# Performance work log

Measured on AMD Instinct MI355X. Metric: run time of the kernel, lower is better.

The kernel has to match this reference:

```python
import jax, jax.numpy as jnp
import numpy as np

B, S, D, KC = 32, 4096, 64, 256  # batch*heads, seq_len, head_dim, compressed dim


def setup_inputs() -> dict:
    key = jax.random.key(0)
    ks = jax.random.split(key, 7)
    return {
        "Q": jax.random.normal(ks[0], (B, S, D), dtype=jnp.float32),
        "K": jax.random.normal(ks[1], (B, S, D), dtype=jnp.float32),
        "V": jax.random.normal(ks[2], (B, S, D), dtype=jnp.float32),
        "E_w": jax.random.normal(ks[3], (KC, S), dtype=jnp.float32) * (1.0 / np.sqrt(S)),
        "E_b": jax.random.normal(ks[4], (KC,), dtype=jnp.float32) * 0.01,
        "F_w": jax.random.normal(ks[5], (KC, S), dtype=jnp.float32) * (1.0 / np.sqrt(S)),
        "F_b": jax.random.normal(ks[6], (KC,), dtype=jnp.float32) * 0.01,
    }


def reference(Q, K, V, E_w, E_b, F_w, F_b):
    # K: [B,S,D] -> transpose -> [B,D,S]; E proj over seq axis -> [B,D,KC]
    Ke = jnp.einsum("bsd,ks->bdk", K, E_w) + E_b  # [B, D, KC]
    # scores: Q @ E(K) -> [B, S, KC], scaled by sqrt(head_dim)
    scale = jnp.sqrt(jnp.asarray(D, dtype=Q.dtype))
    P = jnp.einsum("bsd,bdk->bsk", Q, Ke) / scale
    # causal mask: torch.triu(ones(S, KC)) keeps (i, j) where j >= i
    i = jnp.arange(S)[:, None]
    j = jnp.arange(KC)[None, :]
    keep = j >= i  # [S, KC]
    P = jnp.where(keep[None, :, :], P, jnp.asarray(-1e10, dtype=P.dtype))
    P = jax.nn.softmax(P, axis=-1)  # dropout p=0.0 -> identity
    # V: [B,S,D] -> [B,D,S]; F proj -> [B,D,KC]; transpose -> [B,KC,D]
    Vf = jnp.einsum("bsd,ks->bkd", V, F_w) + F_b[None, :, None]  # [B, KC, D]
    out = jnp.einsum("bsk,bkd->bsd", P, Vf)  # [B, S, D]
    return out
```

## Files before the change

kernel.cpp:

```cpp
#include <hip/hip_runtime.h>
#include <hip/hip_bf16.h>
#include <math.h>

#define NB  32
#define NS  4096
#define ND  64
#define NKC 256
#define ASTR 72
#define PBSTR 264
#define VSTR  264

typedef __attribute__((ext_vector_type(8))) short short8;
typedef __attribute__((ext_vector_type(4))) float f32x4;

__device__ __forceinline__ short f2bf(float f) {
    union { float f; unsigned u; } v; v.f = f;
    return (short)((v.u + 0x7FFFu + ((v.u >> 16) & 1u)) >> 16);
}

__global__ __launch_bounds__(256) void prep(
    const float* __restrict__ Ew, const float* __restrict__ Fw,
    float4* __restrict__ zws, short* __restrict__ EwB, short* __restrict__ FwB)
{
    const int gid = blockIdx.x * 256 + threadIdx.x;
    zws[gid] = (float4){0.f, 0.f, 0.f, 0.f};

    const int half = (NKC * NS) / 8;
    const float* src = (gid < half) ? Ew : Fw;
    short* dst       = (gid < half) ? EwB : FwB;
    const int i8 = (gid < half) ? gid : gid - half;
    float4 a = *(const float4*)&src[(size_t)i8 * 8];
    float4 c = *(const float4*)&src[(size_t)i8 * 8 + 4];
    short8 w;
    w[0] = f2bf(a.x); w[1] = f2bf(a.y); w[2] = f2bf(a.z); w[3] = f2bf(a.w);
    w[4] = f2bf(c.x); w[5] = f2bf(c.y); w[6] = f2bf(c.z); w[7] = f2bf(c.w);
    *(short8*)&dst[(size_t)i8 * 8] = w;
}

template <typename AT>
__global__ __launch_bounds__(256) void proj_gemm(
    const AT* __restrict__ EwX, const AT* __restrict__ FwX,
    const float* __restrict__ K, const float* __restrict__ V,
    float* __restrict__ KeT, float* __restrict__ Vf)
{
    const int x = blockIdx.x, b = blockIdx.y;
    const int chunk = x >> 1, mm = x & 1;
    const AT* __restrict__ Ab    = mm ? FwX : EwX;
    const float* __restrict__ Bg = mm ? V   : K;
    float* __restrict__ Cout     = mm ? Vf  : KeT;

    const int t = threadIdx.x, wave = t >> 6, lane = t & 63;
    const int lm = lane & 15, g = lane >> 4;
    __shared__ short As[256 * ASTR];
    __shared__ short Bs[64 * ASTR];
    const size_t bBase = (size_t)b * NS * ND;
    const int rA = t >> 3, jA = t & 7;
    const int dB = t & 31, sB = t >> 5;

    f32x4 acc[4][4];
#pragma unroll
    for (int mt = 0; mt < 4; ++mt)
#pragma unroll
        for (int nt = 0; nt < 4; ++nt) acc[mt][nt] = (f32x4){0.f, 0.f, 0.f, 0.f};

    const int sBeg = chunk * 512, sEnd = sBeg + 512;
    short8 pa[8];
    float4 paf[16];
    float2 pb[8];
#pragma unroll
    for (int i = 0; i < 8; ++i) {
        if constexpr (sizeof(AT) == 2) {
            pa[i] = *(const short8*)&Ab[(size_t)(i * 32 + rA) * NS + sBeg + jA * 8];
        } else {
            paf[2 * i]     = *(const float4*)&Ab[(size_t)(i * 32 + rA) * NS + sBeg + jA * 8];
            paf[2 * i + 1] = *(const float4*)&Ab[(size_t)(i * 32 + rA) * NS + sBeg + jA * 8 + 4];
        }
    }
#pragma unroll
    for (int i = 0; i < 8; ++i)
        pb[i] = *(const float2*)&Bg[bBase + (size_t)(sBeg + sB * 8 + i) * ND + dB * 2];

    for (int s0 = sBeg; s0 < sEnd; s0 += 64) {
#pragma unroll
        for (int i = 0; i < 8; ++i) {
            if constexpr (sizeof(AT) == 2) {
                *(short8*)&As[(i * 32 + rA) * ASTR + jA * 8] = pa[i];
            } else {
                short8 w;
                w[0] = f2bf(paf[2 * i].x);     w[1] = f2bf(paf[2 * i].y);
                w[2] = f2bf(paf[2 * i].z);     w[3] = f2bf(paf[2 * i].w);
                w[4] = f2bf(paf[2 * i + 1].x); w[5] = f2bf(paf[2 * i + 1].y);
                w[6] = f2bf(paf[2 * i + 1].z); w[7] = f2bf(paf[2 * i + 1].w);
                *(short8*)&As[(i * 32 + rA) * ASTR + jA * 8] = w;
            }
        }
        {
            short8 w0, w1;
#pragma unroll
            for (int i = 0; i < 8; ++i) { w0[i] = f2bf(pb[i].x); w1[i] = f2bf(pb[i].y); }
            *(short8*)&Bs[(dB * 2 + 0) * ASTR + sB * 8] = w0;
            *(short8*)&Bs[(dB * 2 + 1) * ASTR + sB * 8] = w1;
        }
        __syncthreads();
        if (s0 + 64 < sEnd) {
#pragma unroll
            for (int i = 0; i < 8; ++i) {
                if constexpr (sizeof(AT) == 2) {
                    pa[i] = *(const short8*)&Ab[(size_t)(i * 32 + rA) * NS + s0 + 64 + jA * 8];
                } else {
                    paf[2 * i]     = *(const float4*)&Ab[(size_t)(i * 32 + rA) * NS + s0 + 64 + jA * 8];
                    paf[2 * i + 1] = *(const float4*)&Ab[(size_t)(i * 32 + rA) * NS + s0 + 64 + jA * 8 + 4];
                }
            }
#pragma unroll
            for (int i = 0; i < 8; ++i)
                pb[i] = *(const float2*)&Bg[bBase + (size_t)(s0 + 64 + sB * 8 + i) * ND + dB * 2];
        }
#pragma unroll
        for (int ks = 0; ks < 64; ks += 32) {
            short8 aF[4];
#pragma unroll
            for (int mt = 0; mt < 4; ++mt)
                aF[mt] = *(const short8*)&As[(mt * 64 + wave * 16 + lm) * ASTR + ks + g * 8];
#pragma unroll
            for (int nt = 0; nt < 4; ++nt) {
                short8 bF = *(const short8*)&Bs[(nt * 16 + lm) * ASTR + ks + g * 8];
#pragma unroll
                for (int mt = 0; mt < 4; ++mt)
                    acc[mt][nt] = __builtin_amdgcn_mfma_f32_16x16x32_bf16(aF[mt], bF, acc[mt][nt], 0, 0, 0);
            }
        }
        __syncthreads();
    }
#pragma unroll
    for (int mt = 0; mt < 4; ++mt)
#pragma unroll
        for (int r = 0; r < 4; ++r) {
            int kc = mt * 64 + wave * 16 + g * 4 + r;
#pragma unroll
            for (int nt = 0; nt < 4; ++nt)
                atomicAdd(&Cout[((size_t)b * NKC + kc) * ND + nt * 16 + lm], acc[mt][nt][r]);
        }
}

__global__ __launch_bounds__(256) void attn_fused(
    const float* __restrict__ Q,  const float* __restrict__ KeT,
    const float* __restrict__ Vf, const float* __restrict__ Eb,
    const float* __restrict__ Fb, float* __restrict__ out)
{
    const int x = blockIdx.x, b = blockIdx.y, t = threadIdx.x;

    if (x >= 8) {
        __shared__ float pq[16][64];
        __shared__ float mv[64];
        const int kg = t >> 4, dq = t & 15;
        float4 s4 = (float4){0.f, 0.f, 0.f, 0.f};
        for (int p = 0; p < 16; ++p) {
            int k = p * 16 + kg;
            float4 v = *(const float4*)&Vf[((size_t)b * NKC + k) * ND + dq * 4];
            float fb = Fb[k];
            s4.x += v.x + fb; s4.y += v.y + fb; s4.z += v.z + fb; s4.w += v.w + fb;
        }
        *(float4*)&pq[kg][dq * 4] = s4;
        __syncthreads();
        if (t < 64) {
            float m = 0.f;
#pragma unroll
            for (int i = 0; i < 16; ++i) m += pq[i][t];
            mv[t] = m * (1.f / 256.f);
        }
        __syncthreads();
        const int r0 = 256 + (x - 8) * 64;
#pragma unroll
        for (int i = 0; i < 4; ++i) {
            int idx = i * 256 + t, row = idx >> 4, q = idx & 15;
            *(float4*)&out[((size_t)b * NS + r0 + row) * ND + q * 4] =
                *(const float4*)&mv[q * 4];
        }
        return;
    }

    const int s0 = x * 32;
    const int wave = t >> 6, lane = t & 63, lm = lane & 15, g = lane >> 4;
    __shared__ short Qs[32 * ASTR];
    __shared__ short PsB[32 * PBSTR];
    __shared__ short VfT[64 * VSTR];
    __shared__ float rsums[32][4];

    {
        int row = t >> 3, dq = t & 7;
        size_t off = ((size_t)b * NS + s0 + row) * ND + dq * 8;
        float4 q0 = *(const float4*)&Q[off], q1 = *(const float4*)&Q[off + 4];
        short8 w;
        w[0] = f2bf(q0.x); w[1] = f2bf(q0.y); w[2] = f2bf(q0.z); w[3] = f2bf(q0.w);
        w[4] = f2bf(q1.x); w[5] = f2bf(q1.y); w[6] = f2bf(q1.z); w[7] = f2bf(q1.w);
        *(short8*)&Qs[row * ASTR + dq * 8] = w;
    }
    {
        const int dB = t & 31, sB = t >> 5;
#pragma unroll
        for (int pass = 0; pass < 4; ++pass) {
            int kb = pass * 64 + sB * 8;
            float2 v[8]; float fb[8];
#pragma unroll
            for (int i = 0; i < 8; ++i) {
                v[i]  = *(const float2*)&Vf[((size_t)b * NKC + kb + i) * ND + dB * 2];
                fb[i] = Fb[kb + i];
            }
            short8 w0, w1;
#pragma unroll
            for (int i = 0; i < 8; ++i) {
                w0[i] = f2bf(v[i].x + fb[i]);
                w1[i] = f2bf(v[i].y + fb[i]);
            }
            *(short8*)&VfT[(dB * 2 + 0) * VSTR + kb] = w0;
            *(short8*)&VfT[(dB * 2 + 1) * VSTR + kb] = w1;
        }
    }
    __syncthreads();

    f32x4 accP[2][4];
#pragma unroll
    for (int rt = 0; rt < 2; ++rt)
#pragma unroll
        for (int kk = 0; kk < 4; ++kk) accP[rt][kk] = (f32x4){0.f, 0.f, 0.f, 0.f};
#pragma unroll
    for (int kk = 0; kk < 4; ++kk) {
        int kt = wave * 4 + kk;
        float ebv = Eb[kt * 16 + lm];
#pragma unroll
        for (int ks2 = 0; ks2 < 2; ++ks2) {
            const float* kp = &KeT[((size_t)b * NKC + kt * 16 + lm) * ND + ks2 * 32 + g * 8];
            float4 c0 = *(const float4*)kp, c1 = *(const float4*)(kp + 4);
            short8 bf;
            bf[0] = f2bf(c0.x + ebv); bf[1] = f2bf(c0.y + ebv);
            bf[2] = f2bf(c0.z + ebv); bf[3] = f2bf(c0.w + ebv);
            bf[4] = f2bf(c1.x + ebv); bf[5] = f2bf(c1.y + ebv);
            bf[6] = f2bf(c1.z + ebv); bf[7] = f2bf(c1.w + ebv);
#pragma unroll
            for (int rt = 0; rt < 2; ++rt) {
                short8 aq = *(const short8*)&Qs[(rt * 16 + lm) * ASTR + ks2 * 32 + g * 8];
                accP[rt][kk] = __builtin_amdgcn_mfma_f32_16x16x32_bf16(aq, bf, accP[rt][kk], 0, 0, 0);
            }
        }
    }
#pragma unroll
    for (int rt = 0; rt < 2; ++rt)
#pragma unroll
        for (int r = 0; r < 4; ++r) {
            float s = 0.f;
            int rowg = s0 + rt * 16 + g * 4 + r;
#pragma unroll
            for (int kk = 0; kk < 4; ++kk) {
                int col = wave * 64 + kk * 16 + lm;
                float e = (col >= rowg) ? __expf(accP[rt][kk][r] * 0.125f) : 0.f;
                accP[rt][kk][r] = e;
                s += e;
            }
#pragma unroll
            for (int off = 1; off <= 8; off <<= 1) s += __shfl_xor(s, off, 64);
            if (lm == 0) rsums[rt * 16 + g * 4 + r][wave] = s;
        }
    __syncthreads();
#pragma unroll
    for (int rt = 0; rt < 2; ++rt)
#pragma unroll
        for (int r = 0; r < 4; ++r) {
            float4 rs = *(const float4*)&rsums[rt * 16 + g * 4 + r][0];
            float inv = 1.f / (rs.x + rs.y + rs.z + rs.w);
#pragma unroll
            for (int kk = 0; kk < 4; ++kk)
                PsB[(rt * 16 + g * 4 + r) * PBSTR + wave * 64 + kk * 16 + lm] =
                    f2bf(accP[rt][kk][r] * inv);
        }
    __syncthreads();

    f32x4 oa[2];
    oa[0] = (f32x4){0.f, 0.f, 0.f, 0.f};
    oa[1] = (f32x4){0.f, 0.f, 0.f, 0.f};
    for (int ks = x; ks < 8; ++ks) {
        short8 bv = *(const short8*)&VfT[(wave * 16 + lm) * VSTR + ks * 32 + g * 8];
#pragma unroll
        for (int rt = 0; rt < 2; ++rt) {
            short8 av = *(const short8*)&PsB[(rt * 16 + lm) * PBSTR + ks * 32 + g * 8];
            oa[rt] = __builtin_amdgcn_mfma_f32_16x16x32_bf16(av, bv, oa[rt], 0, 0, 0);
        }
    }
#pragma unroll
    for (int rt = 0; rt < 2; ++rt)
#pragma unroll
        for (int r = 0; r < 4; ++r)
            out[((size_t)b * NS + s0 + rt * 16 + g * 4 + r) * ND + wave * 16 + lm] = oa[rt][r];
}

extern "C" void kernel_launch(void* const* d_in, const int* in_sizes, int n_in,
                              void* d_out, int out_size, void* d_ws, size_t ws_size,
                              hipStream_t stream) {
    (void)in_sizes; (void)n_in; (void)out_size;
    const float* Q  = (const float*)d_in[0];
    const float* K  = (const float*)d_in[1];
    const float* V  = (const float*)d_in[2];
    const float* Ew = (const float*)d_in[3];
    const float* Eb = (const float*)d_in[4];
    const float* Fw = (const float*)d_in[5];
    const float* Fb = (const float*)d_in[6];
    float* out = (float*)d_out;

    const size_t nKe = (size_t)NB * NKC * ND;
    float* KeT = (float*)d_ws;
    float* Vf  = KeT + nKe;

    if (ws_size >= 8u * 1024 * 1024) {
        short* EwB = (short*)(Vf + nKe);
        short* FwB = EwB + (size_t)NKC * NS;
        prep<<<dim3(1024), 256, 0, stream>>>(Ew, Fw, (float4*)d_ws, EwB, FwB);
        proj_gemm<short><<<dim3(16, NB), 256, 0, stream>>>(EwB, FwB, K, V, KeT, Vf);
    } else {
        hipMemsetAsync(d_ws, 0, 2 * nKe * sizeof(float), stream);
        proj_gemm<float><<<dim3(16, NB), 256, 0, stream>>>(Ew, Fw, K, V, KeT, Vf);
    }
    attn_fused<<<dim3(68, NB), 256, 0, stream>>>(Q, KeT, Vf, Eb, Fb, out);
}
```

Before: 179.3 us.

## Split projection GEMM by M-half and replace atomics with partial-sum reduction

Drops the separate bf16 pre-conversion kernel and memset, converting E_w/F_w to bf16 on the fly inside the projection GEMM. The GEMM grid is doubled by splitting the 256 compressed rows into two halves, and each block writes plain partial sums (staged in the output buffer) instead of issuing atomicAdds. A new reduce kernel sums the 8 sequence-chunk partials into KeT/Vf. This removes atomic contention and a launch, and raises occupancy with launch_bounds(256,4). In exchange it re-reads fp32 weights in every batch block and adds a partial-buffer write/read pass.

New measurement: 181.0 us. Within noise of the previous version (+1.0%).

```diff
diff --git a/kernel.cpp b/kernel.cpp
--- a/kernel.cpp
+++ b/kernel.cpp
@@ -18,63 +18,39 @@
     return (short)((v.u + 0x7FFFu + ((v.u >> 16) & 1u)) >> 16);
 }
 
-__global__ __launch_bounds__(256) void prep(
+__global__ __launch_bounds__(256, 4) void proj_gemm(
     const float* __restrict__ Ew, const float* __restrict__ Fw,
-    float4* __restrict__ zws, short* __restrict__ EwB, short* __restrict__ FwB)
+    const float* __restrict__ K,  const float* __restrict__ V,
+    float* __restrict__ part)
 {
-    const int gid = blockIdx.x * 256 + threadIdx.x;
-    zws[gid] = (float4){0.f, 0.f, 0.f, 0.f};
-
-    const int half = (NKC * NS) / 8;
-    const float* src = (gid < half) ? Ew : Fw;
-    short* dst       = (gid < half) ? EwB : FwB;
-    const int i8 = (gid < half) ? gid : gid - half;
-    float4 a = *(const float4*)&src[(size_t)i8 * 8];
-    float4 c = *(const float4*)&src[(size_t)i8 * 8 + 4];
-    short8 w;
-    w[0] = f2bf(a.x); w[1] = f2bf(a.y); w[2] = f2bf(a.z); w[3] = f2bf(a.w);
-    w[4] = f2bf(c.x); w[5] = f2bf(c.y); w[6] = f2bf(c.z); w[7] = f2bf(c.w);
-    *(short8*)&dst[(size_t)i8 * 8] = w;
-}
-
-template <typename AT>
-__global__ __launch_bounds__(256) void proj_gemm(
-    const AT* __restrict__ EwX, const AT* __restrict__ FwX,
-    const float* __restrict__ K, const float* __restrict__ V,
-    float* __restrict__ KeT, float* __restrict__ Vf)
-{
-    const int x = blockIdx.x, b = blockIdx.y;
+    const int x = blockIdx.x, y = blockIdx.y;
     const int chunk = x >> 1, mm = x & 1;
-    const AT* __restrict__ Ab    = mm ? FwX : EwX;
-    const float* __restrict__ Bg = mm ? V   : K;
-    float* __restrict__ Cout     = mm ? Vf  : KeT;
+    const int b = y >> 1, mhalf = y & 1;
+    const float* __restrict__ A  = (mm ? Fw : Ew) + (size_t)(mhalf * 128) * NS;
+    const float* __restrict__ Bg = mm ? V : K;
+    float* __restrict__ Pout = part + ((size_t)x * 32 + b) * 16384 + mhalf * 8192;
 
     const int t = threadIdx.x, wave = t >> 6, lane = t & 63;
     const int lm = lane & 15, g = lane >> 4;
-    __shared__ short As[256 * ASTR];
+    __shared__ short As[128 * ASTR];
     __shared__ short Bs[64 * ASTR];
     const size_t bBase = (size_t)b * NS * ND;
     const int rA = t >> 3, jA = t & 7;
     const int dB = t & 31, sB = t >> 5;
 
-    f32x4 acc[4][4];
-#pragma unroll
-    for (int mt = 0; mt < 4; ++mt)
+    f32x4 acc[2][4];
+#pragma unroll
+    for (int mt = 0; mt < 2; ++mt)
 #pragma unroll
         for (int nt = 0; nt < 4; ++nt) acc[mt][nt] = (f32x4){0.f, 0.f, 0.f, 0.f};
 
     const int sBeg = chunk * 512, sEnd = sBeg + 512;
-    short8 pa[8];
-    float4 paf[16];
+    float4 paf[8];
     float2 pb[8];
 #pragma unroll
-    for (int i = 0; i < 8; ++i) {
-        if constexpr (sizeof(AT) == 2) {
-            pa[i] = *(const short8*)&Ab[(size_t)(i * 32 + rA) * NS + sBeg + jA * 8];
-        } else {
-            paf[2 * i]     = *(const float4*)&Ab[(size_t)(i * 32 + rA) * NS + sBeg + jA * 8];
-            paf[2 * i + 1] = *(const float4*)&Ab[(size_t)(i * 32 + rA) * NS + sBeg + jA * 8 + 4];
-        }
+    for (int i = 0; i < 4; ++i) {
+        paf[2 * i]     = *(const float4*)&A[(size_t)(i * 32 + rA) * NS + sBeg + jA * 8];
+        paf[2 * i + 1] = *(const float4*)&A[(size_t)(i * 32 + rA) * NS + sBeg + jA * 8 + 4];
     }
 #pragma unroll
     for (int i = 0; i < 8; ++i)
@@ -82,17 +58,13 @@
 
     for (int s0 = sBeg; s0 < sEnd; s0 += 64) {
 #pragma unroll
-        for (int i = 0; i < 8; ++i) {
-            if constexpr (sizeof(AT) == 2) {
-                *(short8*)&As[(i * 32 + rA) * ASTR + jA * 8] = pa[i];
-            } else {
-                short8 w;
-                w[0] = f2bf(paf[2 * i].x);     w[1] = f2bf(paf[2 * i].y);
-                w[2] = f2bf(paf[2 * i].z);     w[3] = f2bf(paf[2 * i].w);
-                w[4] = f2bf(paf[2 * i + 1].x); w[5] = f2bf(paf[2 * i + 1].y);
-                w[6] = f2bf(paf[2 * i + 1].z); w[7] = f2bf(paf[2 * i + 1].w);
-                *(short8*)&As[(i * 32 + rA) * ASTR + jA * 8] = w;
-            }
+        for (int i = 0; i < 4; ++i) {
+            short8 w;
+            w[0] = f2bf(paf[2 * i].x);     w[1] = f2bf(paf[2 * i].y);
+            w[2] = f2bf(paf[2 * i].z);     w[3] = f2bf(paf[2 * i].w);
+            w[4] = f2bf(paf[2 * i + 1].x); w[5] = f2bf(paf[2 * i + 1].y);
+            w[6] = f2bf(paf[2 * i + 1].z); w[7] = f2bf(paf[2 * i + 1].w);
+            *(short8*)&As[(i * 32 + rA) * ASTR + jA * 8] = w;
         }
         {
             short8 w0, w1;
@@ -104,13 +76,9 @@
         __syncthreads();
         if (s0 + 64 < sEnd) {
 #pragma unroll
-            for (int i = 0; i < 8; ++i) {
-                if constexpr (sizeof(AT) == 2) {
-                    pa[i] = *(const short8*)&Ab[(size_t)(i * 32 + rA) * NS + s0 + 64 + jA * 8];
-                } else {
-                    paf[2 * i]     = *(const float4*)&Ab[(size_t)(i * 32 + rA) * NS + s0 + 64 + jA * 8];
-                    paf[2 * i + 1] = *(const float4*)&Ab[(size_t)(i * 32 + rA) * NS + s0 + 64 + jA * 8 + 4];
-                }
+            for (int i = 0; i < 4; ++i) {
+                paf[2 * i]     = *(const float4*)&A[(size_t)(i * 32 + rA) * NS + s0 + 64 + jA * 8];
+                paf[2 * i + 1] = *(const float4*)&A[(size_t)(i * 32 + rA) * NS + s0 + 64 + jA * 8 + 4];
             }
 #pragma unroll
             for (int i = 0; i < 8; ++i)
@@ -118,29 +86,54 @@
         }
 #pragma unroll
         for (int ks = 0; ks < 64; ks += 32) {
-            short8 aF[4];
-#pragma unroll
-            for (int mt = 0; mt < 4; ++mt)
+            short8 aF[2];
+#pragma unroll
+            for (int mt = 0; mt < 2; ++mt)
                 aF[mt] = *(const short8*)&As[(mt * 64 + wave * 16 + lm) * ASTR + ks + g * 8];
 #pragma unroll
             for (int nt = 0; nt < 4; ++nt) {
                 short8 bF = *(const short8*)&Bs[(nt * 16 + lm) * ASTR + ks + g * 8];
 #pragma unroll
-                for (int mt = 0; mt < 4; ++mt)
+                for (int mt = 0; mt < 2; ++mt)
                     acc[mt][nt] = __builtin_amdgcn_mfma_f32_16x16x32_bf16(aF[mt], bF, acc[mt][nt], 0, 0, 0);
             }
         }
         __syncthreads();
     }
 #pragma unroll
-    for (int mt = 0; mt < 4; ++mt)
+    for (int mt = 0; mt < 2; ++mt)
 #pragma unroll
         for (int r = 0; r < 4; ++r) {
-            int kc = mt * 64 + wave * 16 + g * 4 + r;
+            int kcl = mt * 64 + wave * 16 + g * 4 + r;
 #pragma unroll
             for (int nt = 0; nt < 4; ++nt)
-                atomicAdd(&Cout[((size_t)b * NKC + kc) * ND + nt * 16 + lm], acc[mt][nt][r]);
-        }
+                Pout[kcl * 64 + nt * 16 + lm] = acc[mt][nt][r];
+        }
+}
+
+__global__ __launch_bounds__(256) void reduce_part(
+    const float* __restrict__ part, float* __restrict__ KeT, float* __restrict__ Vf)
+{
+    const int x = blockIdx.x, y = blockIdx.y, t = threadIdx.x;
+    const int b = y >> 1, mm = y & 1;
+    float* __restrict__ Out = (mm ? Vf : KeT) + (size_t)b * NKC * ND;
+
+    const int kc = x * 32 + (t >> 3);
+    const int dO = (t & 7) * 8;
+    const int mhalf = kc >> 7, kcl = kc & 127;
+    const size_t inner = (size_t)mhalf * 8192 + kcl * 64 + dO;
+
+    float4 s0 = (float4){0.f, 0.f, 0.f, 0.f};
+    float4 s1 = (float4){0.f, 0.f, 0.f, 0.f};
+#pragma unroll
+    for (int c = 0; c < 8; ++c) {
+        const float* p = part + ((size_t)(c * 2 + mm) * 32 + b) * 16384 + inner;
+        float4 a = *(const float4*)p, bb = *(const float4*)(p + 4);
+        s0.x += a.x;  s0.y += a.y;  s0.z += a.z;  s0.w += a.w;
+        s1.x += bb.x; s1.y += bb.y; s1.z += bb.z; s1.w += bb.w;
+    }
+    *(float4*)&Out[(size_t)kc * 64 + dO]     = s0;
+    *(float4*)&Out[(size_t)kc * 64 + dO + 4] = s1;
 }
 
 __global__ __launch_bounds__(256) void attn_fused(
@@ -296,7 +289,7 @@
 extern "C" void kernel_launch(void* const* d_in, const int* in_sizes, int n_in,
                               void* d_out, int out_size, void* d_ws, size_t ws_size,
                               hipStream_t stream) {
-    (void)in_sizes; (void)n_in; (void)out_size;
+    (void)in_sizes; (void)n_in; (void)out_size; (void)ws_size;
     const float* Q  = (const float*)d_in[0];
     const float* K  = (const float*)d_in[1];
     const float* V  = (const float*)d_in[2];
@@ -310,14 +303,7 @@
     float* KeT = (float*)d_ws;
     float* Vf  = KeT + nKe;
 
-    if (ws_size >= 8u * 1024 * 1024) {
-        short* EwB = (short*)(Vf + nKe);
-        short* FwB = EwB + (size_t)NKC * NS;
-        prep<<<dim3(1024), 256, 0, stream>>>(Ew, Fw, (float4*)d_ws, EwB, FwB);
-        proj_gemm<short><<<dim3(16, NB), 256, 0, stream>>>(EwB, FwB, K, V, KeT, Vf);
-    } else {
-        hipMemsetAsync(d_ws, 0, 2 * nKe * sizeof(float), stream);
-        proj_gemm<float><<<dim3(16, NB), 256, 0, stream>>>(Ew, Fw, K, V, KeT, Vf);
-    }
+    proj_gemm<<<dim3(16, 64), 256, 0, stream>>>(Ew, Fw, K, V, out);
+    reduce_part<<<dim3(8, 64), 256, 0, stream>>>(out, KeT, Vf);
     attn_fused<<<dim3(68, NB), 256, 0, stream>>>(Q, KeT, Vf, Eb, Fb, out);
 }
```
